# Optimization experiments

Measured on AMD Instinct MI355X. Metric: run time of the kernel, lower is better.

## Reference

```python
import jax, jax.numpy as jnp
import numpy as np

B, S, D, H, A = 2, 2048, 1024, 16, 64
INIT_STD = 0.02


def setup_inputs() -> dict:
    key = jax.random.key(0)
    ks = jax.random.split(key, 5)
    return {
        "residual": jax.random.normal(ks[0], (B, S, D), dtype=jnp.float32),
        "Wq": jax.random.normal(ks[1], (H, D, A), dtype=jnp.float32) * INIT_STD,
        "Wk": jax.random.normal(ks[2], (H, D, A), dtype=jnp.float32) * INIT_STD,
        "Wv": jax.random.normal(ks[3], (H, D, A), dtype=jnp.float32) * INIT_STD,
        "Wo": jax.random.normal(ks[4], (H, A, D), dtype=jnp.float32) * INIT_STD,
        "bq": jnp.zeros((H, A), dtype=jnp.float32),
        "bk": jnp.zeros((H, A), dtype=jnp.float32),
        "bv": jnp.zeros((H, A), dtype=jnp.float32),
        "bo": jnp.zeros((D,), dtype=jnp.float32),
    }


def reference(residual, Wq, Wk, Wv, Wo, bq, bk, bv, bo):
    # residual: [B,S,D]; W{q,k,v}: [H,D,A]; Wo: [H,A,D]
    q = jnp.einsum("bsd,hda->bhsa", residual, Wq) + bq[None, :, None, :]
    k = jnp.einsum("bsd,hda->bhsa", residual, Wk) + bk[None, :, None, :]
    v = jnp.einsum("bsd,hda->bhsa", residual, Wv) + bv[None, :, None, :]
    scale = 1.0 / jnp.sqrt(jnp.float32(q.shape[-1]))
    scores = jnp.einsum("bhsa,bhta->bhst", q, k) * scale  # [B,H,S,S]
    s = scores.shape[-1]
    causal = jnp.tril(jnp.ones((s, s), dtype=bool))  # True = keep
    # original masked_fill with -100000.0 (not -inf); stay faithful
    masked = jnp.where(causal, scores, jnp.float32(-100000.0))
    pattern = jax.nn.softmax(masked, axis=-1)
    z = jnp.einsum("bhst,bhta->bshа".replace("а", "a"), pattern, v)  # [B,S,H,A]
    out = jnp.einsum("bsha,had->bsd", z, Wo) + bo
    return out
```

## Files before the change

kernel.cpp:

```cpp
#include <hip/hip_runtime.h>
#include <hip/hip_bf16.h>

#define B_ 2
#define S_ 2048
#define D_ 1024
#define H_ 16
#define A_ 64

typedef __attribute__((ext_vector_type(8))) short bf16x8;
typedef __attribute__((ext_vector_type(4))) float f32x4;
typedef __attribute__((ext_vector_type(4))) unsigned int u32x4;
typedef __attribute__((ext_vector_type(2))) unsigned int u32x2;

#define QSCALE 0.1803368801111204f
#define SMAX 8.0f

__device__ inline short f2bf(float f) {
    union { float f; unsigned u; } x; x.f = f;
    unsigned r = x.u + 0x7fff + ((x.u >> 16) & 1);
    return (short)(r >> 16);
}

__device__ __forceinline__ void gld16(const short* g, short* l) {
    __builtin_amdgcn_global_load_lds(
        (const __attribute__((address_space(1))) unsigned int*)g,
        (__attribute__((address_space(3))) unsigned int*)l, 16, 0, 0);
}

__device__ inline unsigned cvt_pk_bf16(float lo, float hi) {
    unsigned r;
    asm("v_cvt_pk_bf16_f32 %0, %1, %2" : "=v"(r) : "v"(lo), "v"(hi));
    return r;
}
__device__ inline void pl32swap(unsigned &a, unsigned &b) {
    u32x2 r = __builtin_amdgcn_permlane32_swap(a, b, false, false);
    a = r[0]; b = r[1];
}
__device__ inline void pl16swap(unsigned &a, unsigned &b) {
    u32x2 r = __builtin_amdgcn_permlane16_swap(a, b, false, false);
    a = r[0]; b = r[1];
}
__device__ inline float cross_quad_sum(float x) {
    unsigned a = __builtin_bit_cast(unsigned, x), b = a;
    pl32swap(a, b);
    float y = __builtin_bit_cast(float, a) + __builtin_bit_cast(float, b);
    unsigned c = __builtin_bit_cast(unsigned, y), d = c;
    pl16swap(c, d);
    return __builtin_bit_cast(float, c) + __builtin_bit_cast(float, d);
}

__global__ __launch_bounds__(256) void cast_kernel(const float* __restrict__ x,
                                                   short* __restrict__ y, int n) {
    int i = (blockIdx.x * 256 + threadIdx.x) * 8;
    if (i < n) {
        float4 a = *(const float4*)(x + i);
        float4 b = *(const float4*)(x + i + 4);
        bf16x8 o;
        o[0]=f2bf(a.x); o[1]=f2bf(a.y); o[2]=f2bf(a.z); o[3]=f2bf(a.w);
        o[4]=f2bf(b.x); o[5]=f2bf(b.y); o[6]=f2bf(b.z); o[7]=f2bf(b.w);
        *(bf16x8*)(y + i) = o;
    }
}

__global__ __launch_bounds__(256) void wtrans_kernel(
    const float* __restrict__ Wq, const float* __restrict__ Wk,
    const float* __restrict__ Wv, const float* __restrict__ Wo,
    short* __restrict__ Wt, short* __restrict__ Wot) {
    const int kt = blockIdx.x, yy = blockIdx.y, z = blockIdx.z;
    __shared__ short T[64 * 72];
    const int tid = threadIdx.x;
    const int r = tid >> 2, c0 = (tid & 3) * 16;
    const float* src;
    if (z < 3) {
        const float* W = z == 0 ? Wq : (z == 1 ? Wk : Wv);
        src = &W[yy * (D_ * A_) + (kt * 64 + r) * A_ + c0];
    } else {
        src = &Wo[(kt * 64 + r) * D_ + yy * 64 + c0];
    }
    #pragma unroll
    for (int q = 0; q < 4; q++) {
        float4 f = *(const float4*)(src + q * 4);
        T[r * 72 + c0 + q * 4 + 0] = f2bf(f.x);
        T[r * 72 + c0 + q * 4 + 1] = f2bf(f.y);
        T[r * 72 + c0 + q * 4 + 2] = f2bf(f.z);
        T[r * 72 + c0 + q * 4 + 3] = f2bf(f.w);
    }
    __syncthreads();
    const int a = tid >> 2, kc = (tid & 3) * 16;
    bf16x8 o0, o1;
    #pragma unroll
    for (int j = 0; j < 8; j++) {
        o0[j] = T[(kc + j) * 72 + a];
        o1[j] = T[(kc + 8 + j) * 72 + a];
    }
    const int n_base = (z < 3) ? z * 1024 + yy * 64 : yy * 64;
    short* dst = (z < 3) ? &Wt[(n_base + a) * D_ + kt * 64 + kc]
                         : &Wot[(n_base + a) * D_ + kt * 64 + kc];
    *(bf16x8*)dst = o0;
    *(bf16x8*)(dst + 8) = o1;
}

__global__ __launch_bounds__(256) void qkv_gemm(
    const short* __restrict__ X, const short* __restrict__ Wt,
    const float* __restrict__ bq, const float* __restrict__ bk, const float* __restrict__ bv,
    short* __restrict__ Qb, short* __restrict__ Kb, short* __restrict__ Vt) {
    const int mt = blockIdx.x, nt = blockIdx.y;
    const int m0 = mt * 128, n0 = nt * 128;
    const int sel = n0 >> 10;
    __shared__ short Xl[2][128 * 40], Wl[2][128 * 40];
    const int tid = threadIdx.x, wv = tid >> 6, lane = tid & 63, quad = lane >> 4, l16 = lane & 15;
    const int grow = tid >> 1, gk = (tid & 1) * 16;
    f32x4 acc[4][4] = {};
    bf16x8 xr0, xr1, wr0, wr1;
    {
        const short* xs = &X[(m0 + grow) * D_ + gk];
        xr0 = *(const bf16x8*)xs; xr1 = *(const bf16x8*)(xs + 8);
        const short* wsp = &Wt[(n0 + grow) * D_ + gk];
        wr0 = *(const bf16x8*)wsp; wr1 = *(const bf16x8*)(wsp + 8);
    }
    const int rm = (wv & 1) * 64, cn = (wv >> 1) * 64;
    for (int i = 0; i < 32; i++) {
        const int bu = i & 1;
        *(bf16x8*)&Xl[bu][grow * 40 + gk]     = xr0;
        *(bf16x8*)&Xl[bu][grow * 40 + gk + 8] = xr1;
        *(bf16x8*)&Wl[bu][grow * 40 + gk]     = wr0;
        *(bf16x8*)&Wl[bu][grow * 40 + gk + 8] = wr1;
        __syncthreads();
        if (i < 31) {
            const int k0 = (i + 1) * 32;
            const short* xs = &X[(m0 + grow) * D_ + k0 + gk];
            xr0 = *(const bf16x8*)xs; xr1 = *(const bf16x8*)(xs + 8);
            const short* wsp = &Wt[(n0 + grow) * D_ + k0 + gk];
            wr0 = *(const bf16x8*)wsp; wr1 = *(const bf16x8*)(wsp + 8);
        }
        bf16x8 af[4];
        #pragma unroll
        for (int rt = 0; rt < 4; rt++)
            af[rt] = *(bf16x8*)&Xl[bu][(rm + rt * 16 + l16) * 40 + quad * 8];
        #pragma unroll
        for (int ct = 0; ct < 4; ct++) {
            bf16x8 bf = *(bf16x8*)&Wl[bu][(cn + ct * 16 + l16) * 40 + quad * 8];
            #pragma unroll
            for (int rt = 0; rt < 4; rt++)
                acc[rt][ct] = __builtin_amdgcn_mfma_f32_16x16x32_bf16(af[rt], bf, acc[rt][ct], 0, 0, 0);
        }
    }
    const int b = m0 >> 11;
    const float* bias = sel == 0 ? bq : (sel == 1 ? bk : bv);
    if (sel < 2) {
        short* dst = sel == 0 ? Qb : Kb;
        const float scale = sel == 0 ? QSCALE : 1.0f;
        #pragma unroll
        for (int ct = 0; ct < 4; ct++) {
            const int n = n0 + cn + ct * 16 + l16;
            const int h = (n >> 6) & 15, a = n & 63;
            const float bi = bias[n & 1023];
            #pragma unroll
            for (int rt = 0; rt < 4; rt++)
                #pragma unroll
                for (int r = 0; r < 4; r++) {
                    const int row = m0 + rm + rt * 16 + quad * 4 + r;
                    const int s = row & (S_ - 1);
                    dst[(((b * H_) + h) * S_ + s) * A_ + a] = f2bf((acc[rt][ct][r] + bi) * scale);
                }
        }
    } else {
        #pragma unroll
        for (int ct = 0; ct < 4; ct++) {
            const int n = n0 + cn + ct * 16 + l16;
            const int h = (n >> 6) & 15, a = n & 63;
            const float bi = bias[n & 1023];
            #pragma unroll
            for (int rt = 0; rt < 4; rt++) {
                short4 pk;
                pk.x = f2bf(acc[rt][ct][0] + bi);
                pk.y = f2bf(acc[rt][ct][1] + bi);
                pk.z = f2bf(acc[rt][ct][2] + bi);
                pk.w = f2bf(acc[rt][ct][3] + bi);
                const int row = m0 + rm + rt * 16 + quad * 4;
                const int s = row & (S_ - 1);
                *(short4*)&Vt[(((b * H_) + h) * A_ + a) * S_ + s] = pk;
            }
        }
    }
}

__global__ __launch_bounds__(512, 4) void flash_kernel(
    const short* __restrict__ Qb, const short* __restrict__ Kb,
    const short* __restrict__ Vt, short* __restrict__ Z) {
    const int xx = blockIdx.x, h = blockIdx.y, b = blockIdx.z;
    const int x = (((h >> 3) ^ b) & 1) ? (15 - xx) : xx;
    const int bh = b * H_ + h;
    const int qa = 2 * x, qb = 2 * x + 1;
    __shared__ short Kl[2][4096], Vl[2][4096];
    const int tid = threadIdx.x, wv = tid >> 6, lane = tid & 63, quad = lane >> 4, l16 = lane & 15;
    const int wg = wv & 3;
    const int myqt = (wv < 4) ? qb : qa;
    const int qpos = wg * 16 + l16;

    const int L = tid;
    const int srow = (L >> 7) * 16 + (L & 15);
    const int scol = ((L >> 6) & 1) * 32 + ((L >> 4) & 3) * 8;

    const short* qptr = &Qb[(bh * S_ + myqt * 64 + wg * 16 + l16) * A_ + quad * 8];
    bf16x8 qf[2] = { *(const bf16x8*)qptr, *(const bf16x8*)(qptr + 32) };

    f32x4 O[4] = {};
    float l_i = 0.f;

    const short* kgp = &Kb[(bh * S_ + srow) * A_ + scol];
    const short* vgp = &Vt[(bh * A_ + srow) * S_ + scol];

    gld16(kgp, &Kl[0][L * 8]);
    gld16(vgp, &Vl[0][L * 8]);

    for (int kt = 0; kt <= qb; kt++) {
        const int bu = kt & 1;
        __syncthreads();
        if (kt < qb) {
            gld16(kgp + (kt + 1) * 64 * A_, &Kl[bu ^ 1][L * 8]);
            gld16(vgp + (kt + 1) * 64,      &Vl[bu ^ 1][L * 8]);
        }
        if (kt <= myqt) {
            f32x4 sacc[4] = {};
            #pragma unroll
            for (int kk = 0; kk < 2; kk++)
                #pragma unroll
                for (int ct = 0; ct < 4; ct++) {
                    bf16x8 kf = *(bf16x8*)&Kl[bu][((ct * 2 + kk) * 64 + lane) * 8];
                    sacc[ct] = __builtin_amdgcn_mfma_f32_16x16x32_bf16(kf, qf[kk], sacc[ct], 0, 0, 0);
                }
            if (kt == myqt) {
                #pragma unroll
                for (int ct = 0; ct < 4; ct++)
                    #pragma unroll
                    for (int r = 0; r < 4; r++)
                        if (ct * 16 + quad * 4 + r > qpos) sacc[ct][r] = -1e30f;
            }
            #pragma unroll
            for (int ct = 0; ct < 4; ct++)
                #pragma unroll
                for (int r = 0; r < 4; r++)
                    sacc[ct][r] = exp2f(sacc[ct][r] - SMAX);
            f32x4 ps;
            #pragma unroll
            for (int r = 0; r < 4; r++)
                ps[r] = (sacc[0][r] + sacc[1][r]) + (sacc[2][r] + sacc[3][r]);
            l_i += (ps[0] + ps[1]) + (ps[2] + ps[3]);
            #pragma unroll
            for (int kk = 0; kk < 2; kk++) {
                unsigned A0 = cvt_pk_bf16(sacc[2 * kk][0], sacc[2 * kk][1]);
                unsigned A1 = cvt_pk_bf16(sacc[2 * kk][2], sacc[2 * kk][3]);
                unsigned B0 = cvt_pk_bf16(sacc[2 * kk + 1][0], sacc[2 * kk + 1][1]);
                unsigned B1 = cvt_pk_bf16(sacc[2 * kk + 1][2], sacc[2 * kk + 1][3]);
                pl32swap(A0, B0);
                pl16swap(A0, B0);
                pl32swap(A1, B1);
                pl16swap(A1, B1);
                u32x4 wu; wu[0] = A0; wu[1] = A1; wu[2] = B0; wu[3] = B1;
                bf16x8 pb = __builtin_bit_cast(bf16x8, wu);
                #pragma unroll
                for (int ct = 0; ct < 4; ct++) {
                    bf16x8 vf = *(bf16x8*)&Vl[bu][((ct * 2 + kk) * 64 + lane) * 8];
                    O[ct] = __builtin_amdgcn_mfma_f32_16x16x32_bf16(vf, pb, O[ct], 0, 0, 0);
                }
            }
        }
    }
    const float inv = 1.0f / cross_quad_sum(l_i);
    const int s = myqt * 64 + wg * 16 + l16;
    #pragma unroll
    for (int ct = 0; ct < 4; ct++) {
        short4 o4;
        o4.x = f2bf(O[ct][0] * inv);
        o4.y = f2bf(O[ct][1] * inv);
        o4.z = f2bf(O[ct][2] * inv);
        o4.w = f2bf(O[ct][3] * inv);
        *(short4*)&Z[(b * S_ + s) * (H_ * A_) + h * A_ + ct * 16 + quad * 4] = o4;
    }
}

__global__ __launch_bounds__(256) void proj_gemm(
    const short* __restrict__ Zb, const short* __restrict__ Wot,
    const float* __restrict__ bo, float* __restrict__ out) {
    const int mt = blockIdx.x, nt = blockIdx.y;
    const int m0 = mt * 128, n0 = nt * 64;
    __shared__ short Xl[2][128 * 40], Wl[2][64 * 40];
    const int tid = threadIdx.x, wv = tid >> 6, lane = tid & 63, quad = lane >> 4, l16 = lane & 15;
    const int grow = tid >> 1, gk = (tid & 1) * 16;
    const bool doW = (tid < 128);
    f32x4 acc[4][2] = {};
    bf16x8 xr0, xr1, wr0, wr1;
    {
        const short* xs = &Zb[(m0 + grow) * D_ + gk];
        xr0 = *(const bf16x8*)xs; xr1 = *(const bf16x8*)(xs + 8);
        if (doW) {
            const short* wsp = &Wot[(n0 + grow) * D_ + gk];
            wr0 = *(const bf16x8*)wsp; wr1 = *(const bf16x8*)(wsp + 8);
        }
    }
    const int rm = (wv & 1) * 64, cn = (wv >> 1) * 32;
    for (int i = 0; i < 32; i++) {
        const int bu = i & 1;
        *(bf16x8*)&Xl[bu][grow * 40 + gk]     = xr0;
        *(bf16x8*)&Xl[bu][grow * 40 + gk + 8] = xr1;
        if (doW) {
            *(bf16x8*)&Wl[bu][grow * 40 + gk]     = wr0;
            *(bf16x8*)&Wl[bu][grow * 40 + gk + 8] = wr1;
        }
        __syncthreads();
        if (i < 31) {
            const int k0 = (i + 1) * 32;
            const short* xs = &Zb[(m0 + grow) * D_ + k0 + gk];
            xr0 = *(const bf16x8*)xs; xr1 = *(const bf16x8*)(xs + 8);
            if (doW) {
                const short* wsp = &Wot[(n0 + grow) * D_ + k0 + gk];
                wr0 = *(const bf16x8*)wsp; wr1 = *(const bf16x8*)(wsp + 8);
            }
        }
        bf16x8 af[4];
        #pragma unroll
        for (int rt = 0; rt < 4; rt++)
            af[rt] = *(bf16x8*)&Xl[bu][(rm + rt * 16 + l16) * 40 + quad * 8];
        #pragma unroll
        for (int ct = 0; ct < 2; ct++) {
            bf16x8 bf = *(bf16x8*)&Wl[bu][(cn + ct * 16 + l16) * 40 + quad * 8];
            #pragma unroll
            for (int rt = 0; rt < 4; rt++)
                acc[rt][ct] = __builtin_amdgcn_mfma_f32_16x16x32_bf16(af[rt], bf, acc[rt][ct], 0, 0, 0);
        }
    }
    #pragma unroll
    for (int ct = 0; ct < 2; ct++) {
        const int n = n0 + cn + ct * 16 + l16;
        const float bi = bo[n];
        #pragma unroll
        for (int rt = 0; rt < 4; rt++)
            #pragma unroll
            for (int r = 0; r < 4; r++) {
                const int row = m0 + rm + rt * 16 + quad * 4 + r;
                out[row * D_ + n] = acc[rt][ct][r] + bi;
            }
    }
}

extern "C" void kernel_launch(void* const* d_in, const int* in_sizes, int n_in,
                              void* d_out, int out_size, void* d_ws, size_t ws_size,
                              hipStream_t stream) {
    const float* residual = (const float*)d_in[0];
    const float* Wq = (const float*)d_in[1];
    const float* Wk = (const float*)d_in[2];
    const float* Wv = (const float*)d_in[3];
    const float* Wo = (const float*)d_in[4];
    const float* bq = (const float*)d_in[5];
    const float* bk = (const float*)d_in[6];
    const float* bv = (const float*)d_in[7];
    const float* bo = (const float*)d_in[8];
    float* out = (float*)d_out;

    char* ws = (char*)d_ws;
    const size_t NE = (size_t)B_ * S_ * D_;
    short* Xbf = (short*)(ws);
    short* Wt  = (short*)(ws +  8ull * 1024 * 1024);
    short* Wot = (short*)(ws + 14ull * 1024 * 1024);
    short* Qb  = (short*)(ws + 16ull * 1024 * 1024);
    short* Kb  = (short*)(ws + 24ull * 1024 * 1024);
    short* Vt  = (short*)(ws + 32ull * 1024 * 1024);
    short* Zb  = (short*)(ws + 40ull * 1024 * 1024);

    hipLaunchKernelGGL(cast_kernel, dim3((int)(NE / (256 * 8))), dim3(256), 0, stream,
                       residual, Xbf, (int)NE);
    hipLaunchKernelGGL(wtrans_kernel, dim3(16, 16, 4), dim3(256), 0, stream,
                       Wq, Wk, Wv, Wo, Wt, Wot);
    hipLaunchKernelGGL(qkv_gemm, dim3(32, 24), dim3(256), 0, stream,
                       Xbf, Wt, bq, bk, bv, Qb, Kb, Vt);
    hipLaunchKernelGGL(flash_kernel, dim3(16, H_, B_), dim3(512), 0, stream,
                       Qb, Kb, Vt, Zb);
    hipLaunchKernelGGL(proj_gemm, dim3(32, 16), dim3(256), 0, stream,
                       Zb, Wot, bo, out);
}
```

Measured before the change: 209.4 us.

## Stage 128-key tiles through registers instead of direct global-to-LDS loads

The flash attention loop now handles two 64-key subtiles per barrier round, which halves the number of __syncthreads calls. K/V data is prefetched into registers (four 16-byte loads per thread) and written to double-buffered LDS, replacing the async global_load_lds path. LDS use doubles to 64 KB per block, and register pressure rises from the held prefetch values. Both changes can reduce occupancy under the launch bound of 4 blocks of 512 threads.

```diff
diff --git a/kernel.cpp b/kernel.cpp
--- a/kernel.cpp
+++ b/kernel.cpp
@@ -19,12 +19,6 @@
     union { float f; unsigned u; } x; x.f = f;
     unsigned r = x.u + 0x7fff + ((x.u >> 16) & 1);
     return (short)(r >> 16);
-}
-
-__device__ __forceinline__ void gld16(const short* g, short* l) {
-    __builtin_amdgcn_global_load_lds(
-        (const __attribute__((address_space(1))) unsigned int*)g,
-        (__attribute__((address_space(3))) unsigned int*)l, 16, 0, 0);
 }
 
 __device__ inline unsigned cvt_pk_bf16(float lo, float hi) {
@@ -192,7 +186,7 @@
     const int x = (((h >> 3) ^ b) & 1) ? (15 - xx) : xx;
     const int bh = b * H_ + h;
     const int qa = 2 * x, qb = 2 * x + 1;
-    __shared__ short Kl[2][4096], Vl[2][4096];
+    __shared__ short Kl[2][8192], Vl[2][8192];
     const int tid = threadIdx.x, wv = tid >> 6, lane = tid & 63, quad = lane >> 4, l16 = lane & 15;
     const int wg = wv & 3;
     const int myqt = (wv < 4) ? qb : qa;
@@ -210,59 +204,73 @@
 
     const short* kgp = &Kb[(bh * S_ + srow) * A_ + scol];
     const short* vgp = &Vt[(bh * A_ + srow) * S_ + scol];
-
-    gld16(kgp, &Kl[0][L * 8]);
-    gld16(vgp, &Vl[0][L * 8]);
-
-    for (int kt = 0; kt <= qb; kt++) {
-        const int bu = kt & 1;
+    bf16x8 k0 = *(const bf16x8*)(kgp);
+    bf16x8 k1 = *(const bf16x8*)(kgp + 64 * A_);
+    bf16x8 v0 = *(const bf16x8*)(vgp);
+    bf16x8 v1 = *(const bf16x8*)(vgp + 64);
+
+    const int R = x + 1;
+    for (int rnd = 0; rnd < R; rnd++) {
+        const int bu = rnd & 1;
+        *(bf16x8*)&Kl[bu][L * 8]        = k0;
+        *(bf16x8*)&Kl[bu][4096 + L * 8] = k1;
+        *(bf16x8*)&Vl[bu][L * 8]        = v0;
+        *(bf16x8*)&Vl[bu][4096 + L * 8] = v1;
         __syncthreads();
-        if (kt < qb) {
-            gld16(kgp + (kt + 1) * 64 * A_, &Kl[bu ^ 1][L * 8]);
-            gld16(vgp + (kt + 1) * 64,      &Vl[bu ^ 1][L * 8]);
-        }
-        if (kt <= myqt) {
-            f32x4 sacc[4] = {};
-            #pragma unroll
-            for (int kk = 0; kk < 2; kk++)
-                #pragma unroll
-                for (int ct = 0; ct < 4; ct++) {
-                    bf16x8 kf = *(bf16x8*)&Kl[bu][((ct * 2 + kk) * 64 + lane) * 8];
-                    sacc[ct] = __builtin_amdgcn_mfma_f32_16x16x32_bf16(kf, qf[kk], sacc[ct], 0, 0, 0);
+        if (rnd < R - 1) {
+            const int o = (rnd + 1) * 128;
+            k0 = *(const bf16x8*)(kgp + o * A_);
+            k1 = *(const bf16x8*)(kgp + (o + 64) * A_);
+            v0 = *(const bf16x8*)(vgp + o);
+            v1 = *(const bf16x8*)(vgp + o + 64);
+        }
+        #pragma unroll
+        for (int sub = 0; sub < 2; sub++) {
+            const int ksub = 2 * rnd + sub;
+            if (ksub <= myqt) {
+                const int sb = sub * 4096;
+                f32x4 sacc[4] = {};
+                #pragma unroll
+                for (int kk = 0; kk < 2; kk++)
+                    #pragma unroll
+                    for (int ct = 0; ct < 4; ct++) {
+                        bf16x8 kf = *(bf16x8*)&Kl[bu][sb + ((ct * 2 + kk) * 64 + lane) * 8];
+                        sacc[ct] = __builtin_amdgcn_mfma_f32_16x16x32_bf16(kf, qf[kk], sacc[ct], 0, 0, 0);
+                    }
+                if (ksub == myqt) {
+                    #pragma unroll
+                    for (int ct = 0; ct < 4; ct++)
+                        #pragma unroll
+                        for (int r = 0; r < 4; r++)
+                            if (ct * 16 + quad * 4 + r > qpos) sacc[ct][r] = -1e30f;
                 }
-            if (kt == myqt) {
                 #pragma unroll
                 for (int ct = 0; ct < 4; ct++)
                     #pragma unroll
                     for (int r = 0; r < 4; r++)
-                        if (ct * 16 + quad * 4 + r > qpos) sacc[ct][r] = -1e30f;
-            }
-            #pragma unroll
-            for (int ct = 0; ct < 4; ct++)
+                        sacc[ct][r] = exp2f(sacc[ct][r] - SMAX);
+                f32x4 ps;
                 #pragma unroll
                 for (int r = 0; r < 4; r++)
-                    sacc[ct][r] = exp2f(sacc[ct][r] - SMAX);
-            f32x4 ps;
-            #pragma unroll
-            for (int r = 0; r < 4; r++)
-                ps[r] = (sacc[0][r] + sacc[1][r]) + (sacc[2][r] + sacc[3][r]);
-            l_i += (ps[0] + ps[1]) + (ps[2] + ps[3]);
-            #pragma unroll
-            for (int kk = 0; kk < 2; kk++) {
-                unsigned A0 = cvt_pk_bf16(sacc[2 * kk][0], sacc[2 * kk][1]);
-                unsigned A1 = cvt_pk_bf16(sacc[2 * kk][2], sacc[2 * kk][3]);
-                unsigned B0 = cvt_pk_bf16(sacc[2 * kk + 1][0], sacc[2 * kk + 1][1]);
-                unsigned B1 = cvt_pk_bf16(sacc[2 * kk + 1][2], sacc[2 * kk + 1][3]);
-                pl32swap(A0, B0);
-                pl16swap(A0, B0);
-                pl32swap(A1, B1);
-                pl16swap(A1, B1);
-                u32x4 wu; wu[0] = A0; wu[1] = A1; wu[2] = B0; wu[3] = B1;
-                bf16x8 pb = __builtin_bit_cast(bf16x8, wu);
-                #pragma unroll
-                for (int ct = 0; ct < 4; ct++) {
-                    bf16x8 vf = *(bf16x8*)&Vl[bu][((ct * 2 + kk) * 64 + lane) * 8];
-                    O[ct] = __builtin_amdgcn_mfma_f32_16x16x32_bf16(vf, pb, O[ct], 0, 0, 0);
+                    ps[r] = (sacc[0][r] + sacc[1][r]) + (sacc[2][r] + sacc[3][r]);
+                l_i += (ps[0] + ps[1]) + (ps[2] + ps[3]);
+                #pragma unroll
+                for (int kk = 0; kk < 2; kk++) {
+                    unsigned A0 = cvt_pk_bf16(sacc[2 * kk][0], sacc[2 * kk][1]);
+                    unsigned A1 = cvt_pk_bf16(sacc[2 * kk][2], sacc[2 * kk][3]);
+                    unsigned B0 = cvt_pk_bf16(sacc[2 * kk + 1][0], sacc[2 * kk + 1][1]);
+                    unsigned B1 = cvt_pk_bf16(sacc[2 * kk + 1][2], sacc[2 * kk + 1][3]);
+                    pl32swap(A0, B0);
+                    pl16swap(A0, B0);
+                    pl32swap(A1, B1);
+                    pl16swap(A1, B1);
+                    u32x4 wu; wu[0] = A0; wu[1] = A1; wu[2] = B0; wu[3] = B1;
+                    bf16x8 pb = __builtin_bit_cast(bf16x8, wu);
+                    #pragma unroll
+                    for (int ct = 0; ct < 4; ct++) {
+                        bf16x8 vf = *(bf16x8*)&Vl[bu][sb + ((ct * 2 + kk) * 64 + lane) * 8];
+                        O[ct] = __builtin_amdgcn_mfma_f32_16x16x32_bf16(vf, pb, O[ct], 0, 0, 0);
+                    }
                 }
             }
         }
```

Result: faster. 191.5 us (-8.5%).
